# Optimization experiments

Hardware: AMD Instinct MI355X
Metric: run time of the kernel (lower is better)

The kernel has to match this reference:

```python
import jax, jax.numpy as jnp
import numpy as np

EPS = 1e-8
LN_EPS = 1e-5
DIM, NHEADS = 512, 8
HEAD_DIM = DIM // NHEADS
SCALE = HEAD_DIM ** -0.5
ROLE_VOCAB = 8


def _layernorm(x, g, b):
    mu = x.mean(-1, keepdims=True)
    var = ((x - mu) ** 2).mean(-1, keepdims=True)
    return (x - mu) * jax.lax.rsqrt(var + LN_EPS) * g + b


def setup_inputs() -> dict:
    key = jax.random.key(0)
    ks = jax.random.split(key, 16)
    B, K, L, D = 8, 4, 1024, DIM
    s = 1.0 / np.sqrt(D)
    return {
        "state_repr": jax.random.normal(ks[0], (B, K, L, D), jnp.float32),
        "residue_mask": jax.random.randint(ks[1], (B, K, L), 0, 2) > 0,
        "state_weights": jax.random.uniform(ks[2], (B, K), jnp.float32),
        "state_roles": jax.random.randint(ks[3], (B, K), 0, ROLE_VOCAB),
        "state_present_mask": jnp.ones((B, K), dtype=bool),
        "role_emb": jax.random.normal(ks[4], (ROLE_VOCAB, D), jnp.float32),
        "Wq": jax.random.normal(ks[5], (D, D), jnp.float32) * s,
        "Wk": jax.random.normal(ks[6], (D, D), jnp.float32) * s,
        "Wv": jax.random.normal(ks[7], (D, D), jnp.float32) * s,
        "Wo": jax.random.normal(ks[8], (D, D), jnp.float32) * s,
        "ln1_g": jnp.ones((3 * D,), jnp.float32),
        "ln1_b": jnp.zeros((3 * D,), jnp.float32),
        "Wg1": jax.random.normal(ks[9], (D, 3 * D), jnp.float32) / np.sqrt(3 * D),
        "bg1": jnp.zeros((D,), jnp.float32),
        "Wg2": jax.random.normal(ks[10], (D, D), jnp.float32) * s,
        "bg2": jnp.zeros((D,), jnp.float32),
        "norm_g": jnp.ones((D,), jnp.float32),
        "norm_b": jnp.zeros((D,), jnp.float32),
    }


def _forward(state_repr, residue_mask, state_weights, state_roles, state_present_mask,
             role_emb, Wq, Wk, Wv, Wo, ln1_g, ln1_b, Wg1, bg1, Wg2, bg2, norm_g, norm_b):
    B, K, L, D = state_repr.shape
    H, hd = NHEADS, HEAD_DIM
    roles = jnp.maximum(state_roles, 0)
    role_e = role_emb[roles][:, :, None, :]                       # [B,K,1,D]
    valid = residue_mask & state_present_mask[:, :, None]          # [B,K,L]

    # normalized state weights
    pres = state_present_mask.astype(jnp.float32)
    w = state_weights.astype(jnp.float32) * pres
    denom = w.sum(1, keepdims=True)
    fallback = pres / jnp.maximum(pres.sum(1, keepdims=True), 1.0)
    nsw = jnp.where(denom > EPS, w / jnp.maximum(denom, EPS), fallback)  # [B,K]

    x = (state_repr + role_e) * valid[..., None]
    x = x.transpose(0, 2, 1, 3)                                    # [B,L,K,D]
    valid_rlk = valid.transpose(0, 2, 1)                           # [B,L,K]

    def proj(W):  # torch Linear: y = x @ W.T
        return (x @ W.T).reshape(B, L, K, H, hd).transpose(0, 1, 3, 2, 4)  # [B,L,H,K,hd]

    q, k, v = proj(Wq), proj(Wk), proj(Wv)
    logits = jnp.einsum('blhqd,blhkd->blhqk', q, k) * SCALE
    logits = logits + jnp.log(jnp.maximum(nsw, EPS))[:, None, None, None, :]
    key_mask = valid_rlk[:, :, None, None, :]                      # [B,L,1,1,K]
    logits = jnp.where(key_mask, logits, -jnp.inf)
    attn = jax.nn.softmax(logits, axis=-1)
    attn = jnp.nan_to_num(attn, nan=0.0, posinf=0.0, neginf=0.0)
    attn_out = jnp.einsum('blhqk,blhkd->blhqd', attn, v)
    attn_out = attn_out.transpose(0, 1, 3, 2, 4).reshape(B, L, K, D)
    attn_out = (attn_out @ Wo.T) * valid_rlk[..., None]

    swr = nsw[:, None, :] * valid_rlk.astype(jnp.float32)          # [B,L,K]
    swr = swr / jnp.maximum(swr.sum(-1, keepdims=True), EPS)
    weighted_mean = jnp.sum(x * swr[..., None], axis=2)            # [B,L,D]
    attn_pooled = jnp.sum(attn_out * swr[..., None], axis=2)

    max_in = jnp.where(valid_rlk[..., None], x, -1e9)
    max_feat = max_in.max(axis=2)
    has_any = valid_rlk.any(axis=2, keepdims=True)
    max_feat = jnp.where(has_any, max_feat, 0.0)

    fusion_base = 0.5 * (attn_pooled + weighted_mean)
    gate_in = jnp.concatenate([attn_pooled, weighted_mean, max_feat], axis=-1)
    h = _layernorm(gate_in, ln1_g, ln1_b)
    h = jax.nn.gelu(h @ Wg1.T + bg1, approximate=False)
    gate = jax.nn.sigmoid(h @ Wg2.T + bg2)
    fused = gate * fusion_base + (1.0 - gate) * max_feat
    fused = _layernorm(fused + weighted_mean, norm_g, norm_b)

    attn_mean = attn.mean(axis=(2, 3))                             # [B,L,K]
    return fused, attn_pooled, weighted_mean, max_feat, attn_mean, nsw


def reference(state_repr, residue_mask, state_weights, state_roles, state_present_mask,
              role_emb, Wq, Wk, Wv, Wo, ln1_g, ln1_b, Wg1, bg1, Wg2, bg2, norm_g, norm_b):
    return _forward(state_repr, residue_mask, state_weights, state_roles, state_present_mask,
                    role_emb, Wq, Wk, Wv, Wo, ln1_g, ln1_b, Wg1, bg1, Wg2, bg2, norm_g, norm_b)
```

## Files before the change

### kernel.cpp

```cpp
#include <hip/hip_runtime.h>
#include <math.h>

#define BB 8
#define KK 4
#define LL 1024
#define DD 512
#define HD 64
#define D3 1536
#define MM (BB*LL*KK)
#define BL (BB*LL)
#define SCALE 0.125f
#define EPSF 1e-8f
#define LN_EPSF 1e-5f

typedef _Float16 hfrag __attribute__((ext_vector_type(8)));
typedef float f32x4 __attribute__((ext_vector_type(4)));

__device__ __forceinline__ unsigned short f2h(float f) {
    _Float16 h = (_Float16)f;
    unsigned short u; __builtin_memcpy(&u, &h, 2); return u;
}
__device__ __forceinline__ float h2f(unsigned short u) {
    _Float16 h; __builtin_memcpy(&h, &u, 2); return (float)h;
}

__device__ __forceinline__ void glds16(const unsigned short* g, unsigned short* l) {
    __builtin_amdgcn_global_load_lds(
        (const __attribute__((address_space(1))) void*)g,
        (__attribute__((address_space(3))) void*)l, 16, 0, 0);
}

__device__ __forceinline__ void nsw_compute(const float* sw, const int* pres,
                                            int b, float* nswv) {
    float w[KK], pr[KK]; float denom = 0.f, ps = 0.f;
    #pragma unroll
    for (int k = 0; k < KK; ++k) {
        pr[k] = pres[b*KK + k] ? 1.f : 0.f;
        w[k]  = sw[b*KK + k] * pr[k];
        denom += w[k]; ps += pr[k];
    }
    #pragma unroll
    for (int k = 0; k < KK; ++k)
        nswv[k] = (denom > EPSF) ? w[k] / fmaxf(denom, EPSF)
                                 : pr[k] / fmaxf(ps, 1.f);
}

#define WSZ 262144
#define OG1 1048576
#define OG2 1835008
#define WTOT 2097152
__global__ __launch_bounds__(256) void cvt_weights(
        const float* __restrict__ Wq, const float* __restrict__ Wk,
        const float* __restrict__ Wv, const float* __restrict__ Wo,
        const float* __restrict__ Wg1, const float* __restrict__ Wg2,
        unsigned short* __restrict__ dst) {
    int t = blockIdx.x * 256 + threadIdx.x;
    int e = t * 4;
    const float* src; int off;
    if      (e < WSZ)    { src = Wq;  off = e; }
    else if (e < 2*WSZ)  { src = Wk;  off = e - WSZ; }
    else if (e < 3*WSZ)  { src = Wv;  off = e - 2*WSZ; }
    else if (e < OG1)    { src = Wo;  off = e - 3*WSZ; }
    else if (e < OG2)    { src = Wg1; off = e - OG1; }
    else                 { src = Wg2; off = e - OG2; }
    float4 v = *(const float4*)(src + off);
    ushort4 o;
    o.x = f2h(v.x); o.y = f2h(v.y); o.z = f2h(v.z); o.w = f2h(v.w);
    *(ushort4*)(dst + e) = o;
}

__global__ __launch_bounds__(256) void buildx_kernel(
        const float* __restrict__ SR, const int* __restrict__ residue,
        const int* __restrict__ pres, const int* __restrict__ roles,
        const float* __restrict__ role_emb, const float* __restrict__ sw,
        unsigned short* __restrict__ Xh, float* __restrict__ rowmask,
        float* __restrict__ out_wm, float* __restrict__ out_mx,
        float* __restrict__ f_nsw) {
    int t  = blockIdx.x * 256 + threadIdx.x;
    int bl = t >> 7;
    int d4 = (t & 127) << 2;
    int b  = bl >> 10, l = bl & 1023;
    float nswv[KK];
    nsw_compute(sw, pres, b, nswv);
    float mk[KK], swr[KK];
    float ssum = 0.f, many = 0.f;
    #pragma unroll
    for (int k = 0; k < KK; ++k) {
        int bk = b*KK + k;
        bool valid = (residue[(size_t)bk*LL + l] != 0) && (pres[bk] != 0);
        mk[k]  = valid ? 1.f : 0.f;
        swr[k] = nswv[k] * mk[k];
        ssum += swr[k]; many += mk[k];
    }
    float inv = 1.f / fmaxf(ssum, EPSF);
    bool hasany = many > 0.5f;
    float wmx = 0.f, wmy = 0.f, wmz = 0.f, wmw = 0.f;
    float mxx = -1e9f, mxy = -1e9f, mxz = -1e9f, mxw = -1e9f;
    #pragma unroll
    for (int k = 0; k < KK; ++k) {
        int bk = b*KK + k;
        int role = roles[bk]; if (role < 0) role = 0;
        float4 sr = *(const float4*)(SR + ((size_t)bk*LL + l)*DD + d4);
        float4 re = *(const float4*)(role_emb + (size_t)role*DD + d4);
        float xx = (sr.x + re.x)*mk[k], xy = (sr.y + re.y)*mk[k];
        float xz = (sr.z + re.z)*mk[k], xw = (sr.w + re.w)*mk[k];
        ushort4 xs; xs.x = f2h(xx); xs.y = f2h(xy); xs.z = f2h(xz); xs.w = f2h(xw);
        *(ushort4*)(Xh + (size_t)(bl*KK + k)*DD + d4) = xs;
        float s = swr[k]*inv;
        wmx = fmaf(xx, s, wmx); wmy = fmaf(xy, s, wmy);
        wmz = fmaf(xz, s, wmz); wmw = fmaf(xw, s, wmw);
        if (mk[k] > 0.5f) {
            mxx = fmaxf(mxx, xx); mxy = fmaxf(mxy, xy);
            mxz = fmaxf(mxz, xz); mxw = fmaxf(mxw, xw);
        }
    }
    if (!hasany) { mxx = mxy = mxz = mxw = 0.f; }
    float4 wmv; wmv.x = wmx; wmv.y = wmy; wmv.z = wmz; wmv.w = wmw;
    float4 mxv; mxv.x = mxx; mxv.y = mxy; mxv.z = mxz; mxv.w = mxw;
    *(float4*)(out_wm + (size_t)bl*DD + d4) = wmv;
    *(float4*)(out_mx + (size_t)bl*DD + d4) = mxv;
    if (d4 == 0) {
        #pragma unroll
        for (int k = 0; k < KK; ++k) rowmask[bl*KK + k] = mk[k];
    }
    if (blockIdx.x == 0 && threadIdx.x < BB*KK) {
        int bb = threadIdx.x >> 2, kk2 = threadIdx.x & 3;
        float nv[KK];
        nsw_compute(sw, pres, bb, nv);
        f_nsw[threadIdx.x] = nv[kk2];
    }
}

__global__ __launch_bounds__(512, 4) void gemm_qkv_8p(
        const unsigned short* __restrict__ A, const unsigned short* __restrict__ W,
        unsigned short* __restrict__ Cbase) {
    __shared__ __align__(16) unsigned short smem[36864];
    const int tid  = threadIdx.x;
    const int wave = tid >> 6, lane = tid & 63;
    const int id = blockIdx.x;
    const int wg = (id & 7) * 192 + (id >> 3);
    const int m0 = (wg / 12) * 256;
    const int n0 = (wg % 12) * 128;
    const int wm = wave >> 1, wn = wave & 1;
    const int fr = lane & 15, q = lane >> 4;
    const int srow = tid >> 2, scc = tid & 3;
    const int sswz = (scc ^ ((srow >> 1) & 3)) << 3;
    const unsigned short* Ag0 = A + (size_t)(m0 + srow)*512 + sswz;
    const unsigned short* Ag1 = Ag0 + (size_t)128*512;
    const unsigned short* Wg0 = W + (size_t)(n0 + srow)*512 + sswz;
    const int lA0 = tid << 3;
    const int lA1 = (tid + 512) << 3;
    int aoff[4], boff[4];
    #pragma unroll
    for (int mf = 0; mf < 4; ++mf) {
        int row = (wm << 6) + (mf << 4) + fr;
        aoff[mf] = (row << 5) + ((q ^ ((row >> 1) & 3)) << 3);
    }
    #pragma unroll
    for (int nf = 0; nf < 4; ++nf) {
        int row = (wn << 6) + (nf << 4) + fr;
        boff[nf] = (row << 5) + ((q ^ ((row >> 1) & 3)) << 3);
    }
    f32x4 acc[4][4] = {};

#define VMWAIT(N) asm volatile("s_waitcnt vmcnt(" #N ")" ::: "memory")
#define STAGE(tt) do { unsigned short* _d = smem + ((tt) % 3) * 12288; \
        const int _ko = (tt) << 5; \
        glds16(Ag0 + _ko, _d + lA0); glds16(Ag1 + _ko, _d + lA1); \
        glds16(Wg0 + _ko, _d + 8192 + lA0); } while (0)
#define MFROW(ai, areg) \
        acc[ai][0] = __builtin_amdgcn_mfma_f32_16x16x32_f16(areg, b0, acc[ai][0], 0, 0, 0); \
        acc[ai][1] = __builtin_amdgcn_mfma_f32_16x16x32_f16(areg, b1, acc[ai][1], 0, 0, 0); \
        acc[ai][2] = __builtin_amdgcn_mfma_f32_16x16x32_f16(areg, b2, acc[ai][2], 0, 0, 0); \
        acc[ai][3] = __builtin_amdgcn_mfma_f32_16x16x32_f16(areg, b3, acc[ai][3], 0, 0, 0);
#define TILE(t, STG, VM) do { \
        const unsigned short* _Ab = smem + ((t) % 3) * 12288; \
        const unsigned short* _Bb = _Ab + 8192; \
        VMWAIT(VM); \
        __builtin_amdgcn_s_barrier(); \
        __builtin_amdgcn_sched_barrier(0); \
        hfrag b0 = *(const hfrag*)(_Bb + boff[0]); \
        hfrag b1 = *(const hfrag*)(_Bb + boff[1]); \
        hfrag b2 = *(const hfrag*)(_Bb + boff[2]); \
        hfrag b3 = *(const hfrag*)(_Bb + boff[3]); \
        hfrag a0_ = *(const hfrag*)(_Ab + aoff[0]); \
        hfrag a1_ = *(const hfrag*)(_Ab + aoff[1]); \
        hfrag a2_ = *(const hfrag*)(_Ab + aoff[2]); \
        hfrag a3_ = *(const hfrag*)(_Ab + aoff[3]); \
        if (STG) STAGE((t) + 2); \
        __builtin_amdgcn_s_setprio(1); \
        MFROW(0, a0_) MFROW(1, a1_) MFROW(2, a2_) MFROW(3, a3_) \
        __builtin_amdgcn_s_setprio(0); \
    } while (0)

    STAGE(0); STAGE(1);
    #pragma unroll
    for (int t = 0; t < 14; ++t) TILE(t, 1, 3);
    TILE(14, 0, 3);
    TILE(15, 0, 0);
#undef TILE
#undef MFROW
#undef STAGE
#undef VMWAIT

    const int gc0 = n0 + (wn << 6);
    const int seg = gc0 >> 9;
    unsigned short* Cs = Cbase + (size_t)seg * ((size_t)MM * 512);
    const int cb = gc0 & 511;
    #pragma unroll
    for (int mf = 0; mf < 4; ++mf) {
        const int grow = m0 + (wm << 6) + (mf << 4) + (q << 2);
        #pragma unroll
        for (int nf = 0; nf < 4; ++nf) {
            const int col = cb + (nf << 4) + fr;
            #pragma unroll
            for (int r = 0; r < 4; ++r)
                Cs[(size_t)(grow + r) * 512 + col] = f2h(acc[mf][nf][r]);
        }
    }
}

__global__ __launch_bounds__(256, 3) void gemm_g1(
        const unsigned short* __restrict__ A, const unsigned short* __restrict__ W,
        unsigned short* __restrict__ C, const float* __restrict__ bias) {
    __shared__ __align__(16) unsigned short smem[24576];
    const int tid  = threadIdx.x;
    const int wave = tid >> 6, lane = tid & 63;
    const int id = blockIdx.x;
    const int wg = (id & 7) * 32 + (id >> 3);
    const int m0 = (wg >> 2) * 128;
    const int n0 = (wg & 3) * 128;
    const int wm = wave >> 1, wn = wave & 1;
    const int fr = lane & 15, q = lane >> 4;
    const int srow = tid >> 2, scc = tid & 3;
    const int sswz = (scc ^ ((srow >> 1) & 3)) << 3;
    const unsigned short* Ag0 = A + (size_t)(m0 + srow)*D3 + sswz;
    const unsigned short* Ag1 = Ag0 + (size_t)64*D3;
    const unsigned short* Wg0 = W + (size_t)(n0 + srow)*D3 + sswz;
    const unsigned short* Wg1p = Wg0 + (size_t)64*D3;
    const int lA0 = tid << 3;
    const int lA1 = (tid + 256) << 3;
    int aoff[4], boff[4];
    #pragma unroll
    for (int mf = 0; mf < 4; ++mf) {
        int row = (wm << 6) + (mf << 4) + fr;
        aoff[mf] = (row << 5) + ((q ^ ((row >> 1) & 3)) << 3);
    }
    #pragma unroll
    for (int nf = 0; nf < 4; ++nf) {
        int row = (wn << 6) + (nf << 4) + fr;
        boff[nf] = (row << 5) + ((q ^ ((row >> 1) & 3)) << 3);
    }
    f32x4 acc[4][4] = {};

#define VMWAIT(N) asm volatile("s_waitcnt vmcnt(" #N ")" ::: "memory")
#define STAGE(tt) do { unsigned short* _d = smem + ((tt) % 3) * 8192; \
        const int _ko = (tt) << 5; \
        glds16(Ag0 + _ko, _d + lA0); glds16(Ag1 + _ko, _d + lA1); \
        glds16(Wg0 + _ko, _d + 4096 + lA0); glds16(Wg1p + _ko, _d + 4096 + lA1); } while (0)
#define MFROW(ai, areg) \
        acc[ai][0] = __builtin_amdgcn_mfma_f32_16x16x32_f16(areg, b0, acc[ai][0], 0, 0, 0); \
        acc[ai][1] = __builtin_amdgcn_mfma_f32_16x16x32_f16(areg, b1, acc[ai][1], 0, 0, 0); \
        acc[ai][2] = __builtin_amdgcn_mfma_f32_16x16x32_f16(areg, b2, acc[ai][2], 0, 0, 0); \
        acc[ai][3] = __builtin_amdgcn_mfma_f32_16x16x32_f16(areg, b3, acc[ai][3], 0, 0, 0);
#define TILE(t, STG, VM) do { \
        const unsigned short* _Ab = smem + ((t) % 3) * 8192; \
        const unsigned short* _Bb = _Ab + 4096; \
        VMWAIT(VM); \
        __builtin_amdgcn_s_barrier(); \
        __builtin_amdgcn_sched_barrier(0); \
        hfrag b0 = *(const hfrag*)(_Bb + boff[0]); \
        hfrag b1 = *(const hfrag*)(_Bb + boff[1]); \
        hfrag b2 = *(const hfrag*)(_Bb + boff[2]); \
        hfrag b3 = *(const hfrag*)(_Bb + boff[3]); \
        hfrag a0_ = *(const hfrag*)(_Ab + aoff[0]); \
        hfrag a1_ = *(const hfrag*)(_Ab + aoff[1]); \
        hfrag a2_ = *(const hfrag*)(_Ab + aoff[2]); \
        hfrag a3_ = *(const hfrag*)(_Ab + aoff[3]); \
        if (STG) STAGE((t) + 2); \
        __builtin_amdgcn_s_setprio(1); \
        MFROW(0, a0_) MFROW(1, a1_) MFROW(2, a2_) MFROW(3, a3_) \
        __builtin_amdgcn_s_setprio(0); \
    } while (0)

    STAGE(0); STAGE(1);
    #pragma unroll 3
    for (int t = 0; t < 46; ++t) TILE(t, 1, 4);
    TILE(46, 0, 4);
    TILE(47, 0, 0);
#undef TILE
#undef MFROW
#undef STAGE
#undef VMWAIT

    #pragma unroll
    for (int mf = 0; mf < 4; ++mf) {
        const int grow = m0 + (wm << 6) + (mf << 4) + (q << 2);
        #pragma unroll
        for (int nf = 0; nf < 4; ++nf) {
            const int col = n0 + (wn << 6) + (nf << 4) + fr;
            const float bv = bias[col];
            #pragma unroll
            for (int r = 0; r < 4; ++r) {
                float v = acc[mf][nf][r] + bv;
                v = 0.5f * v * (1.f + erff(v * 0.70710678118654752f));
                C[(size_t)(grow + r) * 512 + col] = f2h(v);
            }
        }
    }
}

__global__ __launch_bounds__(256) void wo_pool_kernel(
        const unsigned short* __restrict__ A,
        const unsigned short* __restrict__ W,
        const float* __restrict__ sw, const int* __restrict__ pres,
        const float* __restrict__ rmask,
        const float* __restrict__ in_wm, const float* __restrict__ in_mx,
        const float* __restrict__ ln1_g, const float* __restrict__ ln1_b,
        float* __restrict__ out_ap, unsigned short* __restrict__ hin) {
    __shared__ __align__(16) unsigned short As[32*32];
    __shared__ __align__(16) unsigned short Bs[512*32];
    const int tid = threadIdx.x, wave = tid >> 6, lane = tid & 63;
    const int m0 = blockIdx.x * 32;
    const int srow = lane >> 2, scol = (lane & 3) << 3;
    const unsigned short* Ag = A + (size_t)(m0 + wave*16 + srow)*512 + scol;
    unsigned short* Al = As + (wave*16 + srow)*32 + scol;
    const int brow = wave*128 + srow;
    const unsigned short* Wg = W + (size_t)brow*512 + scol;
    unsigned short* Blb = Bs + brow*32 + scol;
    const int q = lane >> 4, frl = lane & 15;
    const int fq = q * 8;
    f32x4 acc[2][8] = {};
    for (int k0 = 0; k0 < 512; k0 += 32) {
        if (wave < 2) glds16(Ag + k0, Al);
        #pragma unroll
        for (int i = 0; i < 8; ++i)
            glds16(Wg + (size_t)i*16*512 + k0, Blb + i*16*32);
        __syncthreads();
        hfrag af[2], bf[8];
        #pragma unroll
        for (int i = 0; i < 2; ++i)
            af[i] = *(const hfrag*)(As + (i*16 + frl)*32 + fq);
        #pragma unroll
        for (int j = 0; j < 8; ++j)
            bf[j] = *(const hfrag*)(Bs + (wave*128 + j*16 + frl)*32 + fq);
        #pragma unroll
        for (int i = 0; i < 2; ++i)
            #pragma unroll
            for (int j = 0; j < 8; ++j)
                acc[i][j] = __builtin_amdgcn_mfma_f32_16x16x32_f16(af[i], bf[j], acc[i][j], 0, 0, 0);
        __syncthreads();
    }
    float* ap_s = (float*)Bs;
    const int bl0 = m0 >> 2;
    const int b = bl0 >> 10;
    float nv[KK];
    nsw_compute(sw, pres, b, nv);
    #pragma unroll
    for (int i = 0; i < 2; ++i) {
        int bl_loc = i*4 + q;
        int blg = bl0 + bl_loc;
        float s4[KK]; float ssum = 0.f;
        #pragma unroll
        for (int k = 0; k < KK; ++k) { s4[k] = nv[k] * rmask[blg*4 + k]; ssum += s4[k]; }
        float inv = 1.f / fmaxf(ssum, EPSF);
        #pragma unroll
        for (int j = 0; j < 8; ++j) {
            float ap = 0.f;
            #pragma unroll
            for (int r = 0; r < KK; ++r) ap = fmaf(s4[r]*inv, acc[i][j][r], ap);
            ap_s[bl_loc*512 + wave*128 + j*16 + frl] = ap;
        }
    }
    __syncthreads();
    const int blq = tid >> 5;
    const int c0  = (tid & 31) * 16;
    const int blg = bl0 + blq;
    float4 ap4[4], wm4[4], mx4[4];
    #pragma unroll
    for (int v = 0; v < 4; ++v) {
        ap4[v] = *(const float4*)(ap_s + blq*512 + c0 + v*4);
        wm4[v] = *(const float4*)(in_wm + (size_t)blg*512 + c0 + v*4);
        mx4[v] = *(const float4*)(in_mx + (size_t)blg*512 + c0 + v*4);
    }
    float s = 0.f, s2 = 0.f;
    #pragma unroll
    for (int c = 0; c < 16; ++c) {
        float ap = ((const float*)ap4)[c];
        float wm = ((const float*)wm4)[c];
        float mx = ((const float*)mx4)[c];
        s += ap + wm + mx; s2 += ap*ap + wm*wm + mx*mx;
    }
    #pragma unroll
    for (int o = 1; o < 32; o <<= 1) {
        s  += __shfl_xor(s,  o, 32);
        s2 += __shfl_xor(s2, o, 32);
    }
    float mu = s * (1.f/(float)D3);
    float var = s2 * (1.f/(float)D3) - mu*mu;
    float rstd = rsqrtf(var + LN_EPSF);
    #pragma unroll
    for (int v = 0; v < 4; ++v)
        *(float4*)(out_ap + (size_t)blg*512 + c0 + v*4) = ap4[v];
    #pragma unroll
    for (int seg = 0; seg < 3; ++seg) {
        const float* src = (seg == 0) ? (const float*)ap4
                         : (seg == 1) ? (const float*)wm4 : (const float*)mx4;
        int gofs = seg*512 + c0;
        #pragma unroll
        for (int v = 0; v < 4; ++v) {
            float4 g4 = *(const float4*)(ln1_g + gofs + v*4);
            float4 b4 = *(const float4*)(ln1_b + gofs + v*4);
            ushort4 o;
            o.x = f2h((src[v*4+0]-mu)*rstd*g4.x + b4.x);
            o.y = f2h((src[v*4+1]-mu)*rstd*g4.y + b4.y);
            o.z = f2h((src[v*4+2]-mu)*rstd*g4.z + b4.z);
            o.w = f2h((src[v*4+3]-mu)*rstd*g4.w + b4.w);
            *(ushort4*)(hin + (size_t)blg*D3 + gofs + v*4) = o;
        }
    }
}

__global__ __launch_bounds__(256) void wg2_final_kernel(
        const unsigned short* __restrict__ A,
        const unsigned short* __restrict__ W,
        const float* __restrict__ bg2,
        const float* __restrict__ in_ap, const float* __restrict__ in_wm,
        const float* __restrict__ in_mx,
        const float* __restrict__ norm_g, const float* __restrict__ norm_b,
        float* __restrict__ fused) {
    __shared__ __align__(16) unsigned short As[16*32];
    __shared__ __align__(16) unsigned short Bs[512*32];
    __shared__ float rs[16*4], rq[16*4];
    const int tid = threadIdx.x, wave = tid >> 6, lane = tid & 63;
    const int m0 = blockIdx.x * 16;
    const int srow = lane >> 2, scol = (lane & 3) << 3;
    const unsigned short* Ag = A + (size_t)(m0 + srow)*512 + scol;
    unsigned short* Al = As + srow*32 + scol;
    const int brow = wave*128 + srow;
    const unsigned short* Wg = W + (size_t)brow*512 + scol;
    unsigned short* Blb = Bs + brow*32 + scol;
    const int q = lane >> 4, frl = lane & 15;
    const int fq = q * 8;
    f32x4 acc[8] = {};
    for (int k0 = 0; k0 < 512; k0 += 32) {
        if (wave == 0) glds16(Ag + k0, Al);
        #pragma unroll
        for (int i = 0; i < 8; ++i)
            glds16(Wg + (size_t)i*16*512 + k0, Blb + i*16*32);
        __syncthreads();
        hfrag af, bf[8];
        af = *(const hfrag*)(As + frl*32 + fq);
        #pragma unroll
        for (int j = 0; j < 8; ++j)
            bf[j] = *(const hfrag*)(Bs + (wave*128 + j*16 + frl)*32 + fq);
        #pragma unroll
        for (int j = 0; j < 8; ++j)
            acc[j] = __builtin_amdgcn_mfma_f32_16x16x32_f16(af, bf[j], acc[j], 0, 0, 0);
        __syncthreads();
    }
    float pre[8][4];
    float s[4] = {}, s2[4] = {};
    #pragma unroll
    for (int j = 0; j < 8; ++j) {
        int col = wave*128 + j*16 + frl;
        float bv = bg2[col];
        #pragma unroll
        for (int r = 0; r < 4; ++r) {
            int row = m0 + q*4 + r;
            float g = 1.f / (1.f + expf(-(acc[j][r] + bv)));
            float ap = in_ap[(size_t)row*512 + col];
            float wm = in_wm[(size_t)row*512 + col];
            float mx = in_mx[(size_t)row*512 + col];
            float p = g*0.5f*(ap + wm) + (1.f - g)*mx + wm;
            pre[j][r] = p;
            s[r] += p; s2[r] += p*p;
        }
    }
    #pragma unroll
    for (int r = 0; r < 4; ++r) {
        #pragma unroll
        for (int o = 1; o < 16; o <<= 1) {
            s[r]  += __shfl_xor(s[r],  o, 64);
            s2[r] += __shfl_xor(s2[r], o, 64);
        }
        if (frl == 0) {
            rs[(q*4+r)*4 + wave] = s[r];
            rq[(q*4+r)*4 + wave] = s2[r];
        }
    }
    __syncthreads();
    float mu[4], rstd[4];
    #pragma unroll
    for (int r = 0; r < 4; ++r) {
        int rl = q*4 + r;
        float ts  = rs[rl*4] + rs[rl*4+1] + rs[rl*4+2] + rs[rl*4+3];
        float tq  = rq[rl*4] + rq[rl*4+1] + rq[rl*4+2] + rq[rl*4+3];
        float m = ts * (1.f/(float)DD);
        float v = tq * (1.f/(float)DD) - m*m;
        mu[r] = m; rstd[r] = rsqrtf(v + LN_EPSF);
    }
    #pragma unroll
    for (int j = 0; j < 8; ++j) {
        int col = wave*128 + j*16 + frl;
        float g = norm_g[col], bb = norm_b[col];
        #pragma unroll
        for (int r = 0; r < 4; ++r) {
            int row = m0 + q*4 + r;
            fused[(size_t)row*512 + col] = (pre[j][r]-mu[r])*rstd[r]*g + bb;
        }
    }
}

__global__ __launch_bounds__(256) void attn_kernel(
        unsigned short* Qb ,
        const unsigned short* __restrict__ Kb, const unsigned short* __restrict__ Vb,
        const float* __restrict__ sw, const int* __restrict__ pres,
        const float* __restrict__ rowmask,
        float* __restrict__ attn_mean_out) {
    __shared__ float att[128];
    __shared__ float lw[KK], mk[KK];
    int bl = blockIdx.x, b = bl >> 10, mb = bl * KK;
    int tid = threadIdx.x;
    if (tid < KK) {
        float nv[KK];
        nsw_compute(sw, pres, b, nv);
        lw[tid] = logf(fmaxf(nv[tid], EPSF));
        mk[tid] = rowmask[mb + tid];
    }
    __syncthreads();
    if (tid < 128) {
        int h = tid >> 4, i = (tid >> 2) & 3, j = tid & 3;
        const unsigned short* qp = Qb + (size_t)(mb + i)*DD + h*HD;
        const unsigned short* kp = Kb + (size_t)(mb + j)*DD + h*HD;
        float s = 0.f;
        #pragma unroll
        for (int c = 0; c < 8; ++c) {
            hfrag qv = *(const hfrag*)(qp + c*8);
            hfrag kv = *(const hfrag*)(kp + c*8);
            #pragma unroll
            for (int e = 0; e < 8; ++e)
                s = fmaf((float)qv[e], (float)kv[e], s);
        }
        float lg = s * SCALE + lw[j];
        att[tid] = (mk[j] > 0.5f) ? lg : -INFINITY;
    }
    __syncthreads();
    if (tid < 32) {
        int base = tid * 4;
        float l0 = att[base], l1 = att[base+1], l2 = att[base+2], l3 = att[base+3];
        float m = fmaxf(fmaxf(l0, l1), fmaxf(l2, l3));
        if (m == -INFINITY) {
            att[base] = att[base+1] = att[base+2] = att[base+3] = 0.f;
        } else {
            float e0 = expf(l0 - m), e1 = expf(l1 - m), e2 = expf(l2 - m), e3 = expf(l3 - m);
            float inv = 1.f / (e0 + e1 + e2 + e3);
            att[base] = e0*inv; att[base+1] = e1*inv; att[base+2] = e2*inv; att[base+3] = e3*inv;
        }
    }
    __syncthreads();
    if (tid < KK) {
        float s = 0.f;
        for (int hi = 0; hi < 32; ++hi) s += att[hi*4 + tid];
        attn_mean_out[(size_t)bl*KK + tid] = s * (1.f/32.f);
    }
    #pragma unroll
    for (int p = 0; p < 4; ++p) {
        int idx = p*256 + tid;
        int i = idx >> 8, d2 = (idx & 255) << 1, h = d2 >> 6;
        float s0 = 0.f, s1 = 0.f;
        #pragma unroll
        for (int j = 0; j < KK; ++j) {
            float aj = att[h*16 + i*4 + j];
            ushort2 vv = *(const ushort2*)(Vb + (size_t)(mb + j)*DD + d2);
            s0 = fmaf(aj, h2f(vv.x), s0);
            s1 = fmaf(aj, h2f(vv.y), s1);
        }
        ushort2 o; o.x = f2h(s0); o.y = f2h(s1);
        *(ushort2*)(Qb + (size_t)(mb + i)*DD + d2) = o;
    }
}

extern "C" void kernel_launch(void* const* d_in, const int* in_sizes, int n_in,
                              void* d_out, int out_size, void* d_ws, size_t ws_size,
                              hipStream_t stream) {
    const float* SR      = (const float*)d_in[0];
    const int*   residue = (const int*)d_in[1];
    const float* sw      = (const float*)d_in[2];
    const int*   roles   = (const int*)d_in[3];
    const int*   pres    = (const int*)d_in[4];
    const float* role_emb= (const float*)d_in[5];
    const float* Wq      = (const float*)d_in[6];
    const float* Wk      = (const float*)d_in[7];
    const float* Wv      = (const float*)d_in[8];
    const float* Wo      = (const float*)d_in[9];
    const float* ln1_g   = (const float*)d_in[10];
    const float* ln1_b   = (const float*)d_in[11];
    const float* Wg1     = (const float*)d_in[12];
    const float* bg1     = (const float*)d_in[13];
    const float* Wg2     = (const float*)d_in[14];
    const float* bg2     = (const float*)d_in[15];
    const float* norm_g  = (const float*)d_in[16];
    const float* norm_b  = (const float*)d_in[17];

    float* out = (float*)d_out;
    const size_t BLD = (size_t)BL * DD;
    float* f_fused = out;
    float* f_ap    = out + BLD;
    float* f_wm    = out + 2*BLD;
    float* f_mx    = out + 3*BLD;
    float* f_am    = out + 4*BLD;
    float* f_nsw   = out + 4*BLD + (size_t)BL*KK;

    char* base = (char*)d_ws;
    const size_t MD2 = (size_t)MM * DD * 2;
    unsigned short* Xh = (unsigned short*)(base);
    unsigned short* Qh = (unsigned short*)(base + MD2);
    unsigned short* Kh = (unsigned short*)(base + 2*MD2);
    unsigned short* Vh = (unsigned short*)(base + 3*MD2);
    unsigned short* Wb = (unsigned short*)(base + 4*MD2);
    float* rmask = (float*)(base + 4*MD2 + (size_t)WTOT*2);
    unsigned short* AOh  = Qh;
    unsigned short* Hin  = Vh;
    unsigned short* Hbuf = Xh;
    const unsigned short* Wqkv = Wb;
    const unsigned short* Woh  = Wb + 3*WSZ;
    const unsigned short* Wg1h = Wb + OG1;
    const unsigned short* Wg2h = Wb + OG2;

    dim3 blk(256);

    cvt_weights<<<WTOT/1024, blk, 0, stream>>>(Wq, Wk, Wv, Wo, Wg1, Wg2, Wb);
    buildx_kernel<<<(BL*128)/256, blk, 0, stream>>>(SR, residue, pres, roles, role_emb,
                                                    sw, Xh, rmask, f_wm, f_mx, f_nsw);

    gemm_qkv_8p<<<dim3(1536), dim3(512), 0, stream>>>(Xh, Wqkv, Qh);

    attn_kernel<<<BL, blk, 0, stream>>>(Qh, Kh, Vh, sw, pres, rmask, f_am);

    wo_pool_kernel<<<dim3(MM/32), blk, 0, stream>>>(
        AOh, Woh, sw, pres, rmask, f_wm, f_mx, ln1_g, ln1_b, f_ap, Hin);

    gemm_g1<<<dim3(256), blk, 0, stream>>>(Hin, Wg1h, Hbuf, bg1);

    wg2_final_kernel<<<dim3(BL/16), blk, 0, stream>>>(
        Hbuf, Wg2h, bg2, f_ap, f_wm, f_mx, norm_g, norm_b, f_fused);
}
```

Baseline: 353.7 us.

## Split Wo and Wg2 GEMMs from their layernorm epilogues into tiled pipelined GEMMs

```diff
diff --git a/kernel.cpp b/kernel.cpp
--- a/kernel.cpp
+++ b/kernel.cpp
@@ -220,6 +220,150 @@
     }
 }
 
+__global__ __launch_bounds__(512, 4) void wo_gemm(
+        const unsigned short* __restrict__ A,
+        const unsigned short* __restrict__ W,
+        const float* __restrict__ sw, const int* __restrict__ pres,
+        const float* __restrict__ rmask, float* __restrict__ out_ap) {
+    __shared__ __align__(16) unsigned short smem[36864];
+    const int tid  = threadIdx.x;
+    const int wave = tid >> 6, lane = tid & 63;
+    const int id = blockIdx.x;
+    const int wg = (id & 7) * 64 + (id >> 3);
+    const int m0 = (wg >> 2) * 256;
+    const int n0 = (wg & 3) * 128;
+    const int wm = wave >> 1, wn = wave & 1;
+    const int fr = lane & 15, q = lane >> 4;
+    const int srow = tid >> 2, scc = tid & 3;
+    const int sswz = (scc ^ ((srow >> 1) & 3)) << 3;
+    const unsigned short* Ag0 = A + (size_t)(m0 + srow)*512 + sswz;
+    const unsigned short* Ag1 = Ag0 + (size_t)128*512;
+    const unsigned short* Wg0 = W + (size_t)(n0 + srow)*512 + sswz;
+    const int lA0 = tid << 3;
+    const int lA1 = (tid + 512) << 3;
+    int aoff[4], boff[4];
+    #pragma unroll
+    for (int mf = 0; mf < 4; ++mf) {
+        int row = (wm << 6) + (mf << 4) + fr;
+        aoff[mf] = (row << 5) + ((q ^ ((row >> 1) & 3)) << 3);
+    }
+    #pragma unroll
+    for (int nf = 0; nf < 4; ++nf) {
+        int row = (wn << 6) + (nf << 4) + fr;
+        boff[nf] = (row << 5) + ((q ^ ((row >> 1) & 3)) << 3);
+    }
+    f32x4 acc[4][4] = {};
+
+#define VMWAIT(N) asm volatile("s_waitcnt vmcnt(" #N ")" ::: "memory")
+#define STAGE(tt) do { unsigned short* _d = smem + ((tt) % 3) * 12288; \
+        const int _ko = (tt) << 5; \
+        glds16(Ag0 + _ko, _d + lA0); glds16(Ag1 + _ko, _d + lA1); \
+        glds16(Wg0 + _ko, _d + 8192 + lA0); } while (0)
+#define MFROW(ai, areg) \
+        acc[ai][0] = __builtin_amdgcn_mfma_f32_16x16x32_f16(areg, b0, acc[ai][0], 0, 0, 0); \
+        acc[ai][1] = __builtin_amdgcn_mfma_f32_16x16x32_f16(areg, b1, acc[ai][1], 0, 0, 0); \
+        acc[ai][2] = __builtin_amdgcn_mfma_f32_16x16x32_f16(areg, b2, acc[ai][2], 0, 0, 0); \
+        acc[ai][3] = __builtin_amdgcn_mfma_f32_16x16x32_f16(areg, b3, acc[ai][3], 0, 0, 0);
+#define TILE(t, STG, VM) do { \
+        const unsigned short* _Ab = smem + ((t) % 3) * 12288; \
+        const unsigned short* _Bb = _Ab + 8192; \
+        VMWAIT(VM); \
+        __builtin_amdgcn_s_barrier(); \
+        __builtin_amdgcn_sched_barrier(0); \
+        hfrag b0 = *(const hfrag*)(_Bb + boff[0]); \
+        hfrag b1 = *(const hfrag*)(_Bb + boff[1]); \
+        hfrag b2 = *(const hfrag*)(_Bb + boff[2]); \
+        hfrag b3 = *(const hfrag*)(_Bb + boff[3]); \
+        hfrag a0_ = *(const hfrag*)(_Ab + aoff[0]); \
+        hfrag a1_ = *(const hfrag*)(_Ab + aoff[1]); \
+        hfrag a2_ = *(const hfrag*)(_Ab + aoff[2]); \
+        hfrag a3_ = *(const hfrag*)(_Ab + aoff[3]); \
+        if (STG) STAGE((t) + 2); \
+        __builtin_amdgcn_s_setprio(1); \
+        MFROW(0, a0_) MFROW(1, a1_) MFROW(2, a2_) MFROW(3, a3_) \
+        __builtin_amdgcn_s_setprio(0); \
+    } while (0)
+
+    STAGE(0); STAGE(1);
+    #pragma unroll
+    for (int t = 0; t < 14; ++t) TILE(t, 1, 3);
+    TILE(14, 0, 3);
+    TILE(15, 0, 0);
+#undef TILE
+#undef MFROW
+#undef STAGE
+#undef VMWAIT
+
+    const int b = (m0 >> 2) >> 10;
+    float nv[KK];
+    nsw_compute(sw, pres, b, nv);
+    #pragma unroll
+    for (int mf = 0; mf < 4; ++mf) {
+        const int grow = m0 + (wm << 6) + (mf << 4) + (q << 2);
+        const int bl = grow >> 2;
+        float s4[KK]; float ssum = 0.f;
+        #pragma unroll
+        for (int k = 0; k < KK; ++k) { s4[k] = nv[k] * rmask[bl*4 + k]; ssum += s4[k]; }
+        const float inv = 1.f / fmaxf(ssum, EPSF);
+        #pragma unroll
+        for (int nf = 0; nf < 4; ++nf) {
+            const int col = n0 + (wn << 6) + (nf << 4) + fr;
+            float ap = 0.f;
+            #pragma unroll
+            for (int r = 0; r < KK; ++r) ap = fmaf(s4[r]*inv, acc[mf][nf][r], ap);
+            out_ap[(size_t)bl*512 + col] = ap;
+        }
+    }
+}
+
+__global__ __launch_bounds__(256) void ln1_kernel(
+        const float* __restrict__ ap, const float* __restrict__ wm,
+        const float* __restrict__ mx, const float* __restrict__ g,
+        const float* __restrict__ bvec, unsigned short* __restrict__ hin) {
+    const int bl = blockIdx.x * 4 + (threadIdx.x >> 6);
+    const int lane = threadIdx.x & 63;
+    const int c0 = lane * 8;
+    float4 v[3][2];
+    const float* srcs[3] = { ap + (size_t)bl*512 + c0,
+                             wm + (size_t)bl*512 + c0,
+                             mx + (size_t)bl*512 + c0 };
+    float s = 0.f, s2 = 0.f;
+    #pragma unroll
+    for (int sg = 0; sg < 3; ++sg) {
+        v[sg][0] = *(const float4*)(srcs[sg]);
+        v[sg][1] = *(const float4*)(srcs[sg] + 4);
+        #pragma unroll
+        for (int e = 0; e < 8; ++e) {
+            float x = ((const float*)v[sg])[e];
+            s += x; s2 += x*x;
+        }
+    }
+    #pragma unroll
+    for (int o = 1; o < 64; o <<= 1) {
+        s  += __shfl_xor(s,  o, 64);
+        s2 += __shfl_xor(s2, o, 64);
+    }
+    const float mu = s * (1.f/(float)D3);
+    const float var = s2 * (1.f/(float)D3) - mu*mu;
+    const float rstd = rsqrtf(var + LN_EPSF);
+    #pragma unroll
+    for (int sg = 0; sg < 3; ++sg) {
+        const int gofs = sg*512 + c0;
+        #pragma unroll
+        for (int h = 0; h < 2; ++h) {
+            float4 g4 = *(const float4*)(g + gofs + h*4);
+            float4 b4 = *(const float4*)(bvec + gofs + h*4);
+            const float* sv = (const float*)&v[sg][h];
+            ushort4 o4;
+            o4.x = f2h((sv[0]-mu)*rstd*g4.x + b4.x);
+            o4.y = f2h((sv[1]-mu)*rstd*g4.y + b4.y);
+            o4.z = f2h((sv[2]-mu)*rstd*g4.z + b4.z);
+            o4.w = f2h((sv[3]-mu)*rstd*g4.w + b4.w);
+            *(ushort4*)(hin + (size_t)bl*D3 + gofs + h*4) = o4;
+        }
+    }
+}
+
 __global__ __launch_bounds__(256, 3) void gemm_g1(
         const unsigned short* __restrict__ A, const unsigned short* __restrict__ W,
         unsigned short* __restrict__ C, const float* __restrict__ bias) {
@@ -310,206 +454,134 @@
     }
 }
 
-__global__ __launch_bounds__(256) void wo_pool_kernel(
-        const unsigned short* __restrict__ A,
-        const unsigned short* __restrict__ W,
-        const float* __restrict__ sw, const int* __restrict__ pres,
-        const float* __restrict__ rmask,
-        const float* __restrict__ in_wm, const float* __restrict__ in_mx,
-        const float* __restrict__ ln1_g, const float* __restrict__ ln1_b,
-        float* __restrict__ out_ap, unsigned short* __restrict__ hin) {
-    __shared__ __align__(16) unsigned short As[32*32];
-    __shared__ __align__(16) unsigned short Bs[512*32];
-    const int tid = threadIdx.x, wave = tid >> 6, lane = tid & 63;
-    const int m0 = blockIdx.x * 32;
-    const int srow = lane >> 2, scol = (lane & 3) << 3;
-    const unsigned short* Ag = A + (size_t)(m0 + wave*16 + srow)*512 + scol;
-    unsigned short* Al = As + (wave*16 + srow)*32 + scol;
-    const int brow = wave*128 + srow;
-    const unsigned short* Wg = W + (size_t)brow*512 + scol;
-    unsigned short* Blb = Bs + brow*32 + scol;
-    const int q = lane >> 4, frl = lane & 15;
-    const int fq = q * 8;
-    f32x4 acc[2][8] = {};
-    for (int k0 = 0; k0 < 512; k0 += 32) {
-        if (wave < 2) glds16(Ag + k0, Al);
-        #pragma unroll
-        for (int i = 0; i < 8; ++i)
-            glds16(Wg + (size_t)i*16*512 + k0, Blb + i*16*32);
-        __syncthreads();
-        hfrag af[2], bf[8];
-        #pragma unroll
-        for (int i = 0; i < 2; ++i)
-            af[i] = *(const hfrag*)(As + (i*16 + frl)*32 + fq);
-        #pragma unroll
-        for (int j = 0; j < 8; ++j)
-            bf[j] = *(const hfrag*)(Bs + (wave*128 + j*16 + frl)*32 + fq);
-        #pragma unroll
-        for (int i = 0; i < 2; ++i)
-            #pragma unroll
-            for (int j = 0; j < 8; ++j)
-                acc[i][j] = __builtin_amdgcn_mfma_f32_16x16x32_f16(af[i], bf[j], acc[i][j], 0, 0, 0);
-        __syncthreads();
-    }
-    float* ap_s = (float*)Bs;
-    const int bl0 = m0 >> 2;
-    const int b = bl0 >> 10;
-    float nv[KK];
-    nsw_compute(sw, pres, b, nv);
-    #pragma unroll
-    for (int i = 0; i < 2; ++i) {
-        int bl_loc = i*4 + q;
-        int blg = bl0 + bl_loc;
-        float s4[KK]; float ssum = 0.f;
-        #pragma unroll
-        for (int k = 0; k < KK; ++k) { s4[k] = nv[k] * rmask[blg*4 + k]; ssum += s4[k]; }
-        float inv = 1.f / fmaxf(ssum, EPSF);
-        #pragma unroll
-        for (int j = 0; j < 8; ++j) {
-            float ap = 0.f;
-            #pragma unroll
-            for (int r = 0; r < KK; ++r) ap = fmaf(s4[r]*inv, acc[i][j][r], ap);
-            ap_s[bl_loc*512 + wave*128 + j*16 + frl] = ap;
-        }
-    }
-    __syncthreads();
-    const int blq = tid >> 5;
-    const int c0  = (tid & 31) * 16;
-    const int blg = bl0 + blq;
-    float4 ap4[4], wm4[4], mx4[4];
-    #pragma unroll
-    for (int v = 0; v < 4; ++v) {
-        ap4[v] = *(const float4*)(ap_s + blq*512 + c0 + v*4);
-        wm4[v] = *(const float4*)(in_wm + (size_t)blg*512 + c0 + v*4);
-        mx4[v] = *(const float4*)(in_mx + (size_t)blg*512 + c0 + v*4);
-    }
-    float s = 0.f, s2 = 0.f;
-    #pragma unroll
-    for (int c = 0; c < 16; ++c) {
-        float ap = ((const float*)ap4)[c];
-        float wm = ((const float*)wm4)[c];
-        float mx = ((const float*)mx4)[c];
-        s += ap + wm + mx; s2 += ap*ap + wm*wm + mx*mx;
-    }
-    #pragma unroll
-    for (int o = 1; o < 32; o <<= 1) {
-        s  += __shfl_xor(s,  o, 32);
-        s2 += __shfl_xor(s2, o, 32);
-    }
-    float mu = s * (1.f/(float)D3);
-    float var = s2 * (1.f/(float)D3) - mu*mu;
-    float rstd = rsqrtf(var + LN_EPSF);
-    #pragma unroll
-    for (int v = 0; v < 4; ++v)
-        *(float4*)(out_ap + (size_t)blg*512 + c0 + v*4) = ap4[v];
-    #pragma unroll
-    for (int seg = 0; seg < 3; ++seg) {
-        const float* src = (seg == 0) ? (const float*)ap4
-                         : (seg == 1) ? (const float*)wm4 : (const float*)mx4;
-        int gofs = seg*512 + c0;
-        #pragma unroll
-        for (int v = 0; v < 4; ++v) {
-            float4 g4 = *(const float4*)(ln1_g + gofs + v*4);
-            float4 b4 = *(const float4*)(ln1_b + gofs + v*4);
-            ushort4 o;
-            o.x = f2h((src[v*4+0]-mu)*rstd*g4.x + b4.x);
-            o.y = f2h((src[v*4+1]-mu)*rstd*g4.y + b4.y);
-            o.z = f2h((src[v*4+2]-mu)*rstd*g4.z + b4.z);
-            o.w = f2h((src[v*4+3]-mu)*rstd*g4.w + b4.w);
-            *(ushort4*)(hin + (size_t)blg*D3 + gofs + v*4) = o;
-        }
-    }
-}
-
-__global__ __launch_bounds__(256) void wg2_final_kernel(
+__global__ __launch_bounds__(256, 3) void wg2_gemm(
         const unsigned short* __restrict__ A,
         const unsigned short* __restrict__ W,
         const float* __restrict__ bg2,
         const float* __restrict__ in_ap, const float* __restrict__ in_wm,
-        const float* __restrict__ in_mx,
-        const float* __restrict__ norm_g, const float* __restrict__ norm_b,
-        float* __restrict__ fused) {
-    __shared__ __align__(16) unsigned short As[16*32];
-    __shared__ __align__(16) unsigned short Bs[512*32];
-    __shared__ float rs[16*4], rq[16*4];
-    const int tid = threadIdx.x, wave = tid >> 6, lane = tid & 63;
-    const int m0 = blockIdx.x * 16;
-    const int srow = lane >> 2, scol = (lane & 3) << 3;
-    const unsigned short* Ag = A + (size_t)(m0 + srow)*512 + scol;
-    unsigned short* Al = As + srow*32 + scol;
-    const int brow = wave*128 + srow;
-    const unsigned short* Wg = W + (size_t)brow*512 + scol;
-    unsigned short* Blb = Bs + brow*32 + scol;
-    const int q = lane >> 4, frl = lane & 15;
-    const int fq = q * 8;
-    f32x4 acc[8] = {};
-    for (int k0 = 0; k0 < 512; k0 += 32) {
-        if (wave == 0) glds16(Ag + k0, Al);
-        #pragma unroll
-        for (int i = 0; i < 8; ++i)
-            glds16(Wg + (size_t)i*16*512 + k0, Blb + i*16*32);
-        __syncthreads();
-        hfrag af, bf[8];
-        af = *(const hfrag*)(As + frl*32 + fq);
-        #pragma unroll
-        for (int j = 0; j < 8; ++j)
-            bf[j] = *(const hfrag*)(Bs + (wave*128 + j*16 + frl)*32 + fq);
-        #pragma unroll
-        for (int j = 0; j < 8; ++j)
-            acc[j] = __builtin_amdgcn_mfma_f32_16x16x32_f16(af, bf[j], acc[j], 0, 0, 0);
-        __syncthreads();
-    }
-    float pre[8][4];
-    float s[4] = {}, s2[4] = {};
-    #pragma unroll
-    for (int j = 0; j < 8; ++j) {
-        int col = wave*128 + j*16 + frl;
-        float bv = bg2[col];
-        #pragma unroll
-        for (int r = 0; r < 4; ++r) {
-            int row = m0 + q*4 + r;
-            float g = 1.f / (1.f + expf(-(acc[j][r] + bv)));
-            float ap = in_ap[(size_t)row*512 + col];
-            float wm = in_wm[(size_t)row*512 + col];
-            float mx = in_mx[(size_t)row*512 + col];
-            float p = g*0.5f*(ap + wm) + (1.f - g)*mx + wm;
-            pre[j][r] = p;
-            s[r] += p; s2[r] += p*p;
-        }
-    }
-    #pragma unroll
-    for (int r = 0; r < 4; ++r) {
-        #pragma unroll
-        for (int o = 1; o < 16; o <<= 1) {
-            s[r]  += __shfl_xor(s[r],  o, 64);
-            s2[r] += __shfl_xor(s2[r], o, 64);
-        }
-        if (frl == 0) {
-            rs[(q*4+r)*4 + wave] = s[r];
-            rq[(q*4+r)*4 + wave] = s2[r];
-        }
-    }
-    __syncthreads();
-    float mu[4], rstd[4];
-    #pragma unroll
-    for (int r = 0; r < 4; ++r) {
-        int rl = q*4 + r;
-        float ts  = rs[rl*4] + rs[rl*4+1] + rs[rl*4+2] + rs[rl*4+3];
-        float tq  = rq[rl*4] + rq[rl*4+1] + rq[rl*4+2] + rq[rl*4+3];
-        float m = ts * (1.f/(float)DD);
-        float v = tq * (1.f/(float)DD) - m*m;
-        mu[r] = m; rstd[r] = rsqrtf(v + LN_EPSF);
-    }
-    #pragma unroll
-    for (int j = 0; j < 8; ++j) {
-        int col = wave*128 + j*16 + frl;
-        float g = norm_g[col], bb = norm_b[col];
-        #pragma unroll
-        for (int r = 0; r < 4; ++r) {
-            int row = m0 + q*4 + r;
-            fused[(size_t)row*512 + col] = (pre[j][r]-mu[r])*rstd[r]*g + bb;
-        }
-    }
+        const float* __restrict__ in_mx, float* __restrict__ pre) {
+    __shared__ __align__(16) unsigned short smem[24576];
+    const int tid  = threadIdx.x;
+    const int wave = tid >> 6, lane = tid & 63;
+    const int id = blockIdx.x;
+    const int wg = (id & 7) * 32 + (id >> 3);
+    const int m0 = (wg >> 2) * 128;
+    const int n0 = (wg & 3) * 128;
+    const int wm = wave >> 1, wn = wave & 1;
+    const int fr = lane & 15, q = lane >> 4;
+    const int srow = tid >> 2, scc = tid & 3;
+    const int sswz = (scc ^ ((srow >> 1) & 3)) << 3;
+    const unsigned short* Ag0 = A + (size_t)(m0 + srow)*512 + sswz;
+    const unsigned short* Ag1 = Ag0 + (size_t)64*512;
+    const unsigned short* Wg0 = W + (size_t)(n0 + srow)*512 + sswz;
+    const unsigned short* Wg1p = Wg0 + (size_t)64*512;
+    const int lA0 = tid << 3;
+    const int lA1 = (tid + 256) << 3;
+    int aoff[4], boff[4];
+    #pragma unroll
+    for (int mf = 0; mf < 4; ++mf) {
+        int row = (wm << 6) + (mf << 4) + fr;
+        aoff[mf] = (row << 5) + ((q ^ ((row >> 1) & 3)) << 3);
+    }
+    #pragma unroll
+    for (int nf = 0; nf < 4; ++nf) {
+        int row = (wn << 6) + (nf << 4) + fr;
+        boff[nf] = (row << 5) + ((q ^ ((row >> 1) & 3)) << 3);
+    }
+    f32x4 acc[4][4] = {};
+
+#define VMWAIT(N) asm volatile("s_waitcnt vmcnt(" #N ")" ::: "memory")
+#define STAGE(tt) do { unsigned short* _d = smem + ((tt) % 3) * 8192; \
+        const int _ko = (tt) << 5; \
+        glds16(Ag0 + _ko, _d + lA0); glds16(Ag1 + _ko, _d + lA1); \
+        glds16(Wg0 + _ko, _d + 4096 + lA0); glds16(Wg1p + _ko, _d + 4096 + lA1); } while (0)
+#define MFROW(ai, areg) \
+        acc[ai][0] = __builtin_amdgcn_mfma_f32_16x16x32_f16(areg, b0, acc[ai][0], 0, 0, 0); \
+        acc[ai][1] = __builtin_amdgcn_mfma_f32_16x16x32_f16(areg, b1, acc[ai][1], 0, 0, 0); \
+        acc[ai][2] = __builtin_amdgcn_mfma_f32_16x16x32_f16(areg, b2, acc[ai][2], 0, 0, 0); \
+        acc[ai][3] = __builtin_amdgcn_mfma_f32_16x16x32_f16(areg, b3, acc[ai][3], 0, 0, 0);
+#define TILE(t, STG, VM) do { \
+        const unsigned short* _Ab = smem + ((t) % 3) * 8192; \
+        const unsigned short* _Bb = _Ab + 4096; \
+        VMWAIT(VM); \
+        __builtin_amdgcn_s_barrier(); \
+        __builtin_amdgcn_sched_barrier(0); \
+        hfrag b0 = *(const hfrag*)(_Bb + boff[0]); \
+        hfrag b1 = *(const hfrag*)(_Bb + boff[1]); \
+        hfrag b2 = *(const hfrag*)(_Bb + boff[2]); \
+        hfrag b3 = *(const hfrag*)(_Bb + boff[3]); \
+        hfrag a0_ = *(const hfrag*)(_Ab + aoff[0]); \
+        hfrag a1_ = *(const hfrag*)(_Ab + aoff[1]); \
+        hfrag a2_ = *(const hfrag*)(_Ab + aoff[2]); \
+        hfrag a3_ = *(const hfrag*)(_Ab + aoff[3]); \
+        if (STG) STAGE((t) + 2); \
+        __builtin_amdgcn_s_setprio(1); \
+        MFROW(0, a0_) MFROW(1, a1_) MFROW(2, a2_) MFROW(3, a3_) \
+        __builtin_amdgcn_s_setprio(0); \
+    } while (0)
+
+    STAGE(0); STAGE(1);
+    #pragma unroll
+    for (int t = 0; t < 14; ++t) TILE(t, 1, 4);
+    TILE(14, 0, 4);
+    TILE(15, 0, 0);
+#undef TILE
+#undef MFROW
+#undef STAGE
+#undef VMWAIT
+
+    #pragma unroll
+    for (int mf = 0; mf < 4; ++mf) {
+        const int grow = m0 + (wm << 6) + (mf << 4) + (q << 2);
+        #pragma unroll
+        for (int nf = 0; nf < 4; ++nf) {
+            const int col = n0 + (wn << 6) + (nf << 4) + fr;
+            const float bv = bg2[col];
+            #pragma unroll
+            for (int r = 0; r < 4; ++r) {
+                const int row = grow + r;
+                float g = 1.f / (1.f + expf(-(acc[mf][nf][r] + bv)));
+                float ap = in_ap[(size_t)row*512 + col];
+                float wmv = in_wm[(size_t)row*512 + col];
+                float mxv = in_mx[(size_t)row*512 + col];
+                pre[(size_t)row*512 + col] = g*0.5f*(ap + wmv) + (1.f - g)*mxv + wmv;
+            }
+        }
+    }
+}
+
+__global__ __launch_bounds__(256) void final_ln_kernel(
+        const float* __restrict__ pre, const float* __restrict__ ng,
+        const float* __restrict__ nb, float* __restrict__ fused) {
+    const int row = blockIdx.x * 4 + (threadIdx.x >> 6);
+    const int lane = threadIdx.x & 63;
+    const int c0 = lane * 8;
+    float4 p0 = *(const float4*)(pre + (size_t)row*512 + c0);
+    float4 p1 = *(const float4*)(pre + (size_t)row*512 + c0 + 4);
+    float s = 0.f, s2 = 0.f;
+    const float* pv = (const float*)&p0;
+    #pragma unroll
+    for (int e = 0; e < 4; ++e) { s += pv[e]; s2 += pv[e]*pv[e]; }
+    pv = (const float*)&p1;
+    #pragma unroll
+    for (int e = 0; e < 4; ++e) { s += pv[e]; s2 += pv[e]*pv[e]; }
+    #pragma unroll
+    for (int o = 1; o < 64; o <<= 1) {
+        s  += __shfl_xor(s,  o, 64);
+        s2 += __shfl_xor(s2, o, 64);
+    }
+    const float mu = s * (1.f/(float)DD);
+    const float var = s2 * (1.f/(float)DD) - mu*mu;
+    const float rstd = rsqrtf(var + LN_EPSF);
+    float4 g0 = *(const float4*)(ng + c0), g1 = *(const float4*)(ng + c0 + 4);
+    float4 b0 = *(const float4*)(nb + c0), b1 = *(const float4*)(nb + c0 + 4);
+    float4 o0, o1;
+    o0.x = (p0.x-mu)*rstd*g0.x + b0.x; o0.y = (p0.y-mu)*rstd*g0.y + b0.y;
+    o0.z = (p0.z-mu)*rstd*g0.z + b0.z; o0.w = (p0.w-mu)*rstd*g0.w + b0.w;
+    o1.x = (p1.x-mu)*rstd*g1.x + b1.x; o1.y = (p1.y-mu)*rstd*g1.y + b1.y;
+    o1.z = (p1.z-mu)*rstd*g1.z + b1.z; o1.w = (p1.w-mu)*rstd*g1.w + b1.w;
+    *(float4*)(fused + (size_t)row*512 + c0) = o0;
+    *(float4*)(fused + (size_t)row*512 + c0 + 4) = o1;
 }
 
 __global__ __launch_bounds__(256) void attn_kernel(
@@ -623,6 +695,7 @@
     unsigned short* AOh  = Qh;
     unsigned short* Hin  = Vh;
     unsigned short* Hbuf = Xh;
+    float* preb = (float*)Kh;
     const unsigned short* Wqkv = Wb;
     const unsigned short* Woh  = Wb + 3*WSZ;
     const unsigned short* Wg1h = Wb + OG1;
@@ -638,11 +711,17 @@
 
     attn_kernel<<<BL, blk, 0, stream>>>(Qh, Kh, Vh, sw, pres, rmask, f_am);
 
-    wo_pool_kernel<<<dim3(MM/32), blk, 0, stream>>>(
-        AOh, Woh, sw, pres, rmask, f_wm, f_mx, ln1_g, ln1_b, f_ap, Hin);
+    wo_gemm<<<dim3(512), dim3(512), 0, stream>>>(
+        AOh, Woh, sw, pres, rmask, f_ap);
+
+    ln1_kernel<<<dim3(BL/4), blk, 0, stream>>>(
+        f_ap, f_wm, f_mx, ln1_g, ln1_b, Hin);
 
     gemm_g1<<<dim3(256), blk, 0, stream>>>(Hin, Wg1h, Hbuf, bg1);
 
-    wg2_final_kernel<<<dim3(BL/16), blk, 0, stream>>>(
-        Hbuf, Wg2h, bg2, f_ap, f_wm, f_mx, norm_g, norm_b, f_fused);
-}
+    wg2_gemm<<<dim3(256), blk, 0, stream>>>(
+        Hbuf, Wg2h, bg2, f_ap, f_wm, f_mx, preb);
+
+    final_ln_kernel<<<dim3(BL/4), blk, 0, stream>>>(
+        preb, norm_g, norm_b, f_fused);
+}
```

Measured after the change: 335.2 us. -5.2%, faster.
